# Optimization experiments

Hardware: AMD Instinct MI355X
Metric: run time of the kernel (lower is better)

Reference implementation:

```python
import jax, jax.numpy as jnp
import numpy as np

C = 32
H = 8

def _layernorm(x, scale, bias, eps=1e-5):
    mu = jnp.mean(x, axis=-1, keepdims=True)
    var = jnp.mean(jnp.square(x - mu), axis=-1, keepdims=True)
    return (x - mu) * jax.lax.rsqrt(var + eps) * scale + bias


def setup_inputs() -> dict:
    key = jax.random.key(0)
    ks = jax.random.split(key, 10)
    B, s, i, j = 1, 128, 256, 256
    m = jax.random.normal(ks[0], (B, s, i, C), dtype=jnp.float32)
    z = jax.random.normal(ks[1], (B, i, j, C), dtype=jnp.float32)
    sd = 1.0 / np.sqrt(C)
    return {
        "m": m,
        "z": z,
        "ln_scale": jnp.ones((C,), jnp.float32),
        "ln_bias": jnp.zeros((C,), jnp.float32),
        "lnb_scale": jnp.ones((C,), jnp.float32),
        "lnb_bias": jnp.zeros((C,), jnp.float32),
        "wq": jax.random.normal(ks[2], (C, C * H), jnp.float32) * sd,
        "wk": jax.random.normal(ks[3], (C, C * H), jnp.float32) * sd,
        "wv": jax.random.normal(ks[4], (C, C * H), jnp.float32) * sd,
        "wb": jax.random.normal(ks[5], (C, H), jnp.float32) * sd,
        "wg": jax.random.normal(ks[6], (C, C * H), jnp.float32) * sd,
        "wo": jax.random.normal(ks[7], (C * H, C), jnp.float32) * (1.0 / np.sqrt(C * H)),
        "bo": jnp.zeros((C,), jnp.float32),
    }


def reference(m, z, ln_scale, ln_bias, lnb_scale, lnb_bias, wq, wk, wv, wb, wg, wo, bo):
    B, s, i, _ = m.shape
    j = z.shape[2]
    mn = _layernorm(m, ln_scale, ln_bias)                      # (B,s,i,c)
    q = (mn @ wq).reshape(B, s, i, H, C)                        # (B,s,i,h,c)
    k = (mn @ wk).reshape(B, s, i, H, C)
    v = (mn @ wv).reshape(B, s, i, H, C)
    gate = jax.nn.sigmoid(mn @ wg).reshape(B, s, i, H, C)       # (B,s,i,h,c)
    b = (_layernorm(z, lnb_scale, lnb_bias) @ wb)               # (B,i,j,h)
    a = jnp.einsum('bsihc,bsjhc->bsijh', q, k) * (C ** -0.5) + b[:, None]
    a = jax.nn.softmax(a, axis=-2)                              # softmax over j
    o = gate * jnp.einsum('bsijh,bsjhc->bsihc', a, v)
    o = o.reshape(B, s, i, H * C)
    return o @ wo + bo
```

## Files before the change

kernel.cpp:

```cpp
#include <hip/hip_runtime.h>

constexpr int NC = 32;
constexpr int NH = 8;
constexpr int NS = 128;
constexpr int NI = 256;
constexpr int NJ = 256;
constexpr float LN_EPS = 1e-5f;
constexpr float QSCALE = 0.17677669529663687f;
constexpr float LOG2E  = 1.4426950408889634f;

typedef __bf16 bf16x8 __attribute__((ext_vector_type(8)));
typedef __bf16 bf16x2 __attribute__((ext_vector_type(2)));
typedef float floatx4 __attribute__((ext_vector_type(4)));

__device__ __forceinline__ float fexp2(float x) {
#if __has_builtin(__builtin_amdgcn_exp2f)
    return __builtin_amdgcn_exp2f(x);
#else
    return exp2f(x);
#endif
}
__device__ __forceinline__ float frcp(float x) {
#if __has_builtin(__builtin_amdgcn_rcpf)
    return __builtin_amdgcn_rcpf(x);
#else
    return 1.0f / x;
#endif
}
__device__ __forceinline__ unsigned pk2c(float a, float b) {
    union { bf16x2 v; unsigned u; } c;
    c.v = bf16x2{(__bf16)a, (__bf16)b};
    return c.u;
}

__device__ __forceinline__ int qkOff(int row, int chunk) {
    return row * 32 + ((chunk ^ ((row >> 1) & 3)) << 3);
}
__device__ __forceinline__ int vOff(int c, int chunk) {
    return c * 256 + ((chunk ^ (c & 7)) << 3);
}
__device__ __forceinline__ int pOff(int base, int row, int chunk) {
    return base + row * 32 + ((chunk ^ ((row >> 1) & 3)) << 3);
}

__global__ __launch_bounds__(256) void biasprep_kernel(
    const float* __restrict__ z, const float* __restrict__ lnb_s,
    const float* __restrict__ lnb_b, const float* __restrict__ wb,
    const float* __restrict__ wq, const float* __restrict__ wk,
    const float* __restrict__ wv, const float* __restrict__ wg,
    const float* __restrict__ wo,
    float* __restrict__ bias32, unsigned short* __restrict__ wprep,
    unsigned short* __restrict__ wofrag)
{
    const int b = blockIdx.x;
    const int t = threadIdx.x;
    if (b < 256) {
        const int w_ = b >> 6;
        const int it = (b >> 4) & 3;
        const int jc = (b >> 1) & 7;
        const int jt = b & 1;
        const int lm = (t >> 2) & 15;
        const int lq = t >> 6, r = t & 3;
        const int i = w_ * 64 + it * 16 + lm;
        const int j = jc * 32 + jt * 16 + lq * 4 + r;

        const float4* zr = (const float4*)(z + ((size_t)i * NJ + j) * NC);
        float x[NC];
#pragma unroll
        for (int k = 0; k < 8; ++k) {
            float4 v = zr[k];
            x[4*k] = v.x; x[4*k+1] = v.y; x[4*k+2] = v.z; x[4*k+3] = v.w;
        }
        float mu = 0.f;
#pragma unroll
        for (int c = 0; c < NC; ++c) mu += x[c];
        mu *= (1.0f / NC);
        float var = 0.f;
#pragma unroll
        for (int c = 0; c < NC; ++c) { float d = x[c] - mu; var += d * d; }
        var *= (1.0f / NC);
        float rs = rsqrtf(var + LN_EPS);
        float acc[NH];
#pragma unroll
        for (int h = 0; h < NH; ++h) acc[h] = 0.f;
#pragma unroll
        for (int c = 0; c < NC; ++c) {
            float xn = (x[c] - mu) * rs * lnb_s[c] + lnb_b[c];
#pragma unroll
            for (int h = 0; h < NH; ++h) acc[h] += xn * wb[c * NH + h];
        }
        const int base = jc * 8192 + w_ * 2048 + (jt * 4 + it) * 256 + t;
#pragma unroll
        for (int h = 0; h < NH; ++h)
            bias32[h * 65536 + base] = acc[h] * LOG2E;
    } else if (b < 272) {
        int g = (b - 256) * 256 + t;
        int p  = g >> 10;
        int h  = (g >> 7) & 7;
        int ct = (g >> 6) & 1;
        int l  = g & 63;
        const float* W = (p == 0) ? wq : (p == 1) ? wk : (p == 2) ? wv : wg;
        float scale = (p == 0) ? QSCALE * LOG2E : (p == 3) ? LOG2E : 1.0f;
        int col = 32 * h + 16 * ct + (l & 15);
        int r0  = 8 * (l >> 4);
        float v[8];
#pragma unroll
        for (int e = 0; e < 8; ++e) v[e] = W[(r0 + e) * 256 + col] * scale;
        uint4 u;
        u.x = pk2c(v[0], v[1]); u.y = pk2c(v[2], v[3]);
        u.z = pk2c(v[4], v[5]); u.w = pk2c(v[6], v[7]);
        *(uint4*)&wprep[g * 8] = u;
    } else {
        int g = (b - 272) * 256 + t;
        int tile = g >> 6;
        int l = g & 63;
        int kt = tile >> 1, nt = tile & 1;
        int r0 = kt * 32 + 8 * (l >> 4);
        int col = nt * 16 + (l & 15);
        float v[8];
#pragma unroll
        for (int e = 0; e < 8; ++e) v[e] = wo[(r0 + e) * 32 + col];
        uint4 u;
        u.x = pk2c(v[0], v[1]); u.y = pk2c(v[2], v[3]);
        u.z = pk2c(v[4], v[5]); u.w = pk2c(v[6], v[7]);
        *(uint4*)&wofrag[g * 8] = u;
    }
}

__global__ __launch_bounds__(256, 3) void attn_kernel(
    const float* __restrict__ m, const float* __restrict__ ln_s,
    const float* __restrict__ ln_b,
    const unsigned short* __restrict__ wprep,
    const float* __restrict__ bias32,
    unsigned short* __restrict__ attn16)
{
    __shared__ unsigned short KX[256 * 32];
    __shared__ unsigned short Vt[32 * 256];
    __shared__ unsigned short Pbuf[4 * 2048];

    const int t = threadIdx.x;
    const int h = blockIdx.x & 7;
    const int s = blockIdx.x >> 3;
    const int l = t & 63, w = t >> 6;
    const int lm = l & 15, lq = l >> 4;
    const int ibase = w * 64;
    const int pwb = w * 2048;
    const floatx4 zero = {0.f, 0.f, 0.f, 0.f};

    {
        const float4* mr = (const float4*)(m + ((size_t)s * NI + t) * NC);
        float x[NC];
#pragma unroll
        for (int k = 0; k < 8; ++k) {
            float4 v = mr[k];
            x[4*k] = v.x; x[4*k+1] = v.y; x[4*k+2] = v.z; x[4*k+3] = v.w;
        }
        float mu = 0.f;
#pragma unroll
        for (int c = 0; c < NC; ++c) mu += x[c];
        mu *= (1.0f / NC);
        float var = 0.f;
#pragma unroll
        for (int c = 0; c < NC; ++c) { float d = x[c] - mu; var += d * d; }
        var *= (1.0f / NC);
        float rs = rsqrtf(var + LN_EPS);
#pragma unroll
        for (int k = 0; k < 4; ++k) {
            uint4 u;
            u.x = pk2c((x[8*k+0]-mu)*rs*ln_s[8*k+0]+ln_b[8*k+0],
                       (x[8*k+1]-mu)*rs*ln_s[8*k+1]+ln_b[8*k+1]);
            u.y = pk2c((x[8*k+2]-mu)*rs*ln_s[8*k+2]+ln_b[8*k+2],
                       (x[8*k+3]-mu)*rs*ln_s[8*k+3]+ln_b[8*k+3]);
            u.z = pk2c((x[8*k+4]-mu)*rs*ln_s[8*k+4]+ln_b[8*k+4],
                       (x[8*k+5]-mu)*rs*ln_s[8*k+5]+ln_b[8*k+5]);
            u.w = pk2c((x[8*k+6]-mu)*rs*ln_s[8*k+6]+ln_b[8*k+6],
                       (x[8*k+7]-mu)*rs*ln_s[8*k+7]+ln_b[8*k+7]);
            *(uint4*)&KX[qkOff(t, k)] = u;
        }
    }

    const unsigned short* wp = wprep + ((size_t)h * 128 + l) * 8;
    bf16x8 wfQ[2], wfK[2], wfV[2];
#pragma unroll
    for (int ct = 0; ct < 2; ++ct) {
        wfQ[ct] = *(const bf16x8*)&wp[(0 * 1024 + ct * 64) * 8];
        wfK[ct] = *(const bf16x8*)&wp[(1 * 1024 + ct * 64) * 8];
        wfV[ct] = *(const bf16x8*)&wp[(2 * 1024 + ct * 64) * 8];
    }
    bf16x8 Xb[4];
#pragma unroll
    for (int it = 0; it < 4; ++it)
        Xb[it] = *(const bf16x8*)&KX[qkOff(ibase + it * 16 + lm, lq)];

#pragma unroll
    for (int it = 0; it < 4; ++it)
#pragma unroll
        for (int ct = 0; ct < 2; ++ct) {
            floatx4 d = __builtin_amdgcn_mfma_f32_16x16x32_bf16(wfQ[ct], Xb[it], zero, 0, 0, 0);
            uint2 u; u.x = pk2c(d[0], d[1]); u.y = pk2c(d[2], d[3]);
            int row = ibase + it * 16 + lm;
            *(uint2*)&KX[qkOff(row, 2 * ct + (lq >> 1)) + (lq & 1) * 4] = u;
        }
    bf16x8 Qb[4];
#pragma unroll
    for (int it = 0; it < 4; ++it)
        Qb[it] = *(const bf16x8*)&KX[qkOff(ibase + it * 16 + lm, lq)];

#pragma unroll
    for (int it = 0; it < 4; ++it)
#pragma unroll
        for (int ct = 0; ct < 2; ++ct) {
            floatx4 d = __builtin_amdgcn_mfma_f32_16x16x32_bf16(wfK[ct], Xb[it], zero, 0, 0, 0);
            uint2 u; u.x = pk2c(d[0], d[1]); u.y = pk2c(d[2], d[3]);
            int row = ibase + it * 16 + lm;
            *(uint2*)&KX[qkOff(row, 2 * ct + (lq >> 1)) + (lq & 1) * 4] = u;
        }

#pragma unroll
    for (int jt = 0; jt < 4; ++jt)
#pragma unroll
        for (int ct = 0; ct < 2; ++ct) {
            floatx4 d = __builtin_amdgcn_mfma_f32_16x16x32_bf16(Xb[jt], wfV[ct], zero, 0, 0, 0);
            uint2 u; u.x = pk2c(d[0], d[1]); u.y = pk2c(d[2], d[3]);
            int c = ct * 16 + lm;
            int chunk = 8 * w + 2 * jt + (lq >> 1);
            *(uint2*)&Vt[vOff(c, chunk) + (lq & 1) * 4] = u;
        }

    __syncthreads();

    floatx4 accO[2][4];
#pragma unroll
    for (int ct = 0; ct < 2; ++ct)
#pragma unroll
        for (int it = 0; it < 4; ++it) accO[ct][it] = zero;
    float accLv[4] = {0.f, 0.f, 0.f, 0.f};

    const float* bptr = bias32 + (size_t)h * 65536 + w * 2048 + l * 4;

    for (int jc = 0; jc < 8; ++jc) {
        const float* bj = bptr + jc * 8192;

        floatx4 Cre[4][2];
#pragma unroll
        for (int it = 0; it < 4; ++it) {
            Cre[it][0] = *(const floatx4*)(bj + it * 256);
            Cre[it][1] = *(const floatx4*)(bj + (4 + it) * 256);
        }
        bf16x8 Ka0 = *(const bf16x8*)&KX[qkOff(jc * 32 + lm, lq)];
        bf16x8 Ka1 = *(const bf16x8*)&KX[qkOff(jc * 32 + 16 + lm, lq)];
        bf16x8 Va0 = *(const bf16x8*)&Vt[vOff(lm, 4 * jc + lq)];
        bf16x8 Va1 = *(const bf16x8*)&Vt[vOff(16 + lm, 4 * jc + lq)];

#pragma unroll
        for (int it = 0; it < 4; ++it) {
            const int pb = pwb + it * 512;
            floatx4 S0 = __builtin_amdgcn_mfma_f32_16x16x32_bf16(Ka0, Qb[it], Cre[it][0], 0, 0, 0);
            floatx4 S1 = __builtin_amdgcn_mfma_f32_16x16x32_bf16(Ka1, Qb[it], Cre[it][1], 0, 0, 0);
            float p0 = fexp2(S0[0]), p1 = fexp2(S0[1]);
            float p2 = fexp2(S0[2]), p3 = fexp2(S0[3]);
            float p4 = fexp2(S1[0]), p5 = fexp2(S1[1]);
            float p6 = fexp2(S1[2]), p7 = fexp2(S1[3]);
            accLv[it] += ((p0 + p1) + (p2 + p3)) + ((p4 + p5) + (p6 + p7));
            uint2 u0; u0.x = pk2c(p0, p1); u0.y = pk2c(p2, p3);
            uint2 u1; u1.x = pk2c(p4, p5); u1.y = pk2c(p6, p7);
            *(uint2*)&Pbuf[pOff(pb, lm, 0 + (lq >> 1)) + (lq & 1) * 4] = u0;
            *(uint2*)&Pbuf[pOff(pb, lm, 2 + (lq >> 1)) + (lq & 1) * 4] = u1;
        }

        bf16x8 Pb0 = *(const bf16x8*)&Pbuf[pOff(pwb + 0 * 512, lm, lq)];
        bf16x8 Pb1 = *(const bf16x8*)&Pbuf[pOff(pwb + 1 * 512, lm, lq)];
        bf16x8 Pb2 = *(const bf16x8*)&Pbuf[pOff(pwb + 2 * 512, lm, lq)];
        bf16x8 Pb3 = *(const bf16x8*)&Pbuf[pOff(pwb + 3 * 512, lm, lq)];
        accO[0][0] = __builtin_amdgcn_mfma_f32_16x16x32_bf16(Va0, Pb0, accO[0][0], 0, 0, 0);
        accO[1][0] = __builtin_amdgcn_mfma_f32_16x16x32_bf16(Va1, Pb0, accO[1][0], 0, 0, 0);
        accO[0][1] = __builtin_amdgcn_mfma_f32_16x16x32_bf16(Va0, Pb1, accO[0][1], 0, 0, 0);
        accO[1][1] = __builtin_amdgcn_mfma_f32_16x16x32_bf16(Va1, Pb1, accO[1][1], 0, 0, 0);
        accO[0][2] = __builtin_amdgcn_mfma_f32_16x16x32_bf16(Va0, Pb2, accO[0][2], 0, 0, 0);
        accO[1][2] = __builtin_amdgcn_mfma_f32_16x16x32_bf16(Va1, Pb2, accO[1][2], 0, 0, 0);
        accO[0][3] = __builtin_amdgcn_mfma_f32_16x16x32_bf16(Va0, Pb3, accO[0][3], 0, 0, 0);
        accO[1][3] = __builtin_amdgcn_mfma_f32_16x16x32_bf16(Va1, Pb3, accO[1][3], 0, 0, 0);
    }

    {
        bf16x8 wfG0 = *(const bf16x8*)&wp[(3 * 1024 + 0 * 64) * 8];
        bf16x8 wfG1 = *(const bf16x8*)&wp[(3 * 1024 + 1 * 64) * 8];
#pragma unroll
        for (int it = 0; it < 4; ++it) {
            float L = accLv[it];
            L += __shfl_xor(L, 16, 64);
            L += __shfl_xor(L, 32, 64);
            const float inv = frcp(L);
            floatx4 d0 = __builtin_amdgcn_mfma_f32_16x16x32_bf16(wfG0, Xb[it], zero, 0, 0, 0);
            floatx4 d1 = __builtin_amdgcn_mfma_f32_16x16x32_bf16(wfG1, Xb[it], zero, 0, 0, 0);
            const int tile16 = s * 16 + (w * 4 + it);
            unsigned short* ab = attn16 + ((size_t)(tile16 * 8 + h)) * 512;
            const int lo = lm * 8 + (lq & 1) * 4;
            {
                float o0 = accO[0][it][0] * inv * frcp(1.0f + fexp2(-d0[0]));
                float o1 = accO[0][it][1] * inv * frcp(1.0f + fexp2(-d0[1]));
                float o2 = accO[0][it][2] * inv * frcp(1.0f + fexp2(-d0[2]));
                float o3 = accO[0][it][3] * inv * frcp(1.0f + fexp2(-d0[3]));
                uint2 u; u.x = pk2c(o0, o1); u.y = pk2c(o2, o3);
                *(uint2*)&ab[(0 + (lq >> 1)) * 128 + lo] = u;
            }
            {
                float o0 = accO[1][it][0] * inv * frcp(1.0f + fexp2(-d1[0]));
                float o1 = accO[1][it][1] * inv * frcp(1.0f + fexp2(-d1[1]));
                float o2 = accO[1][it][2] * inv * frcp(1.0f + fexp2(-d1[2]));
                float o3 = accO[1][it][3] * inv * frcp(1.0f + fexp2(-d1[3]));
                uint2 u; u.x = pk2c(o0, o1); u.y = pk2c(o2, o3);
                *(uint2*)&ab[(2 + (lq >> 1)) * 128 + lo] = u;
            }
        }
    }
}

__global__ __launch_bounds__(256) void proj_kernel(
    const unsigned short* __restrict__ attn16,
    const unsigned short* __restrict__ wofrag,
    const float* __restrict__ bo, float* __restrict__ out)
{
    const int t = threadIdx.x;
    const int l = t & 63, w = t >> 6;
    const int lm = l & 15, lq = l >> 4;
    const int row0 = blockIdx.x * 128 + w * 32;
    const int t16 = row0 >> 4;
    const floatx4 zero = {0.f, 0.f, 0.f, 0.f};

    floatx4 acc[2][2];
#pragma unroll
    for (int it = 0; it < 2; ++it)
#pragma unroll
        for (int nt = 0; nt < 2; ++nt) acc[it][nt] = zero;

#pragma unroll 2
    for (int kt = 0; kt < 8; ++kt) {
        bf16x8 a0 = *(const bf16x8*)&attn16[((size_t)((t16 + 0) * 8 + kt)) * 512 + l * 8];
        bf16x8 a1 = *(const bf16x8*)&attn16[((size_t)((t16 + 1) * 8 + kt)) * 512 + l * 8];
        bf16x8 b0 = *(const bf16x8*)&wofrag[((kt * 2 + 0) * 64 + l) * 8];
        bf16x8 b1 = *(const bf16x8*)&wofrag[((kt * 2 + 1) * 64 + l) * 8];
        acc[0][0] = __builtin_amdgcn_mfma_f32_16x16x32_bf16(a0, b0, acc[0][0], 0, 0, 0);
        acc[0][1] = __builtin_amdgcn_mfma_f32_16x16x32_bf16(a0, b1, acc[0][1], 0, 0, 0);
        acc[1][0] = __builtin_amdgcn_mfma_f32_16x16x32_bf16(a1, b0, acc[1][0], 0, 0, 0);
        acc[1][1] = __builtin_amdgcn_mfma_f32_16x16x32_bf16(a1, b1, acc[1][1], 0, 0, 0);
    }

    float bov[2] = {bo[lm], bo[16 + lm]};
#pragma unroll
    for (int it = 0; it < 2; ++it)
#pragma unroll
        for (int nt = 0; nt < 2; ++nt)
#pragma unroll
            for (int r = 0; r < 4; ++r)
                out[(size_t)(row0 + it * 16 + lq * 4 + r) * NC + nt * 16 + lm]
                    = acc[it][nt][r] + bov[nt];
}

extern "C" void kernel_launch(void* const* d_in, const int* in_sizes, int n_in,
                              void* d_out, int out_size, void* d_ws, size_t ws_size,
                              hipStream_t stream) {
    const float* m     = (const float*)d_in[0];
    const float* z     = (const float*)d_in[1];
    const float* ln_s  = (const float*)d_in[2];
    const float* ln_b  = (const float*)d_in[3];
    const float* lnb_s = (const float*)d_in[4];
    const float* lnb_b = (const float*)d_in[5];
    const float* wq    = (const float*)d_in[6];
    const float* wk    = (const float*)d_in[7];
    const float* wv    = (const float*)d_in[8];
    const float* wb    = (const float*)d_in[9];
    const float* wg    = (const float*)d_in[10];
    const float* wo    = (const float*)d_in[11];
    const float* bo    = (const float*)d_in[12];
    float* out = (float*)d_out;

    float* bias32 = (float*)d_ws;
    unsigned short* wprep  = (unsigned short*)((char*)d_ws + (2u << 20));
    unsigned short* wofrag = (unsigned short*)((char*)d_ws + (2u << 20) + 65536);
    unsigned short* attn16 = (unsigned short*)((char*)d_ws + (2u << 20) + 65536 + 16384);

    biasprep_kernel<<<276, 256, 0, stream>>>(z, lnb_s, lnb_b, wb, wq, wk, wv, wg,
                                             wo, bias32, wprep, wofrag);
    attn_kernel<<<NS * NH, 256, 0, stream>>>(m, ln_s, ln_b, wprep, bias32, attn16);
    proj_kernel<<<(NS * NI) / 128, 256, 0, stream>>>(attn16, wofrag, bo, out);
}
```

Measured before the change: 116.8 us.

## Fuse three kernels into one persistent kernel with grid barriers

Replaces the bias-prep, attention and projection launches with a single persistent kernel of 512 blocks that runs the phases back to back, separated by atomic-counter grid barriers. Attention work units are looped over the fixed grid, and the output projection is split so each block handles 64 rows. The aim is to remove kernel launch gaps and tail effects between stages. In exchange it adds a memset launch, spin-wait barrier cost, and occupancy lowered to 2 blocks per SM. It also relies on all 512 blocks being co-resident, otherwise the barrier deadlocks.

```diff
diff --git a/kernel.cpp b/kernel.cpp
--- a/kernel.cpp
+++ b/kernel.cpp
@@ -8,6 +8,7 @@
 constexpr float LN_EPS = 1e-5f;
 constexpr float QSCALE = 0.17677669529663687f;
 constexpr float LOG2E  = 1.4426950408889634f;
+constexpr unsigned GRIDN = 512;
 
 typedef __bf16 bf16x8 __attribute__((ext_vector_type(8)));
 typedef __bf16 bf16x2 __attribute__((ext_vector_type(2)));
@@ -43,26 +44,50 @@
     return base + row * 32 + ((chunk ^ ((row >> 1) & 3)) << 3);
 }
 
-__global__ __launch_bounds__(256) void biasprep_kernel(
-    const float* __restrict__ z, const float* __restrict__ lnb_s,
-    const float* __restrict__ lnb_b, const float* __restrict__ wb,
+__device__ __forceinline__ void grid_barrier(unsigned* ctr) {
+    __syncthreads();
+    if (threadIdx.x == 0) {
+        __threadfence();
+        __hip_atomic_fetch_add(ctr, 1u, __ATOMIC_ACQ_REL, __HIP_MEMORY_SCOPE_AGENT);
+        while (__hip_atomic_load(ctr, __ATOMIC_ACQUIRE, __HIP_MEMORY_SCOPE_AGENT) < GRIDN) {
+            __builtin_amdgcn_s_sleep(2);
+        }
+        __threadfence();
+    }
+    __syncthreads();
+}
+
+__global__ __launch_bounds__(256, 2) void fused_kernel(
+    const float* __restrict__ m, const float* __restrict__ z,
+    const float* __restrict__ ln_s, const float* __restrict__ ln_b,
+    const float* __restrict__ lnb_s, const float* __restrict__ lnb_b,
     const float* __restrict__ wq, const float* __restrict__ wk,
-    const float* __restrict__ wv, const float* __restrict__ wg,
-    const float* __restrict__ wo,
+    const float* __restrict__ wv, const float* __restrict__ wb,
+    const float* __restrict__ wg, const float* __restrict__ wo,
+    const float* __restrict__ bo,
     float* __restrict__ bias32, unsigned short* __restrict__ wprep,
-    unsigned short* __restrict__ wofrag)
+    unsigned short* __restrict__ wofrag, unsigned short* __restrict__ attn16,
+    unsigned* __restrict__ bars, float* __restrict__ out)
 {
-    const int b = blockIdx.x;
+    __shared__ unsigned short KX[256 * 32];
+    __shared__ unsigned short Vt[32 * 256];
+    __shared__ unsigned short Pbuf[4 * 2048];
+
+    const int bid = blockIdx.x;
     const int t = threadIdx.x;
-    if (b < 256) {
-        const int w_ = b >> 6;
-        const int it = (b >> 4) & 3;
-        const int jc = (b >> 1) & 7;
-        const int jt = b & 1;
-        const int lm = (t >> 2) & 15;
-        const int lq = t >> 6, r = t & 3;
-        const int i = w_ * 64 + it * 16 + lm;
-        const int j = jc * 32 + jt * 16 + lq * 4 + r;
+    const int l = t & 63, w = t >> 6;
+    const int lm = l & 15, lq = l >> 4;
+    const floatx4 zero = {0.f, 0.f, 0.f, 0.f};
+
+    if (bid < 256) {
+        const int w_ = bid >> 6;
+        const int it = (bid >> 4) & 3;
+        const int jc = (bid >> 1) & 7;
+        const int jt = bid & 1;
+        const int blm = (t >> 2) & 15;
+        const int blq = t >> 6, br = t & 3;
+        const int i = w_ * 64 + it * 16 + blm;
+        const int j = jc * 32 + jt * 16 + blq * 4 + br;
 
         const float4* zr = (const float4*)(z + ((size_t)i * NJ + j) * NC);
         float x[NC];
@@ -93,16 +118,16 @@
 #pragma unroll
         for (int h = 0; h < NH; ++h)
             bias32[h * 65536 + base] = acc[h] * LOG2E;
-    } else if (b < 272) {
-        int g = (b - 256) * 256 + t;
+    } else if (bid < 272) {
+        int g = (bid - 256) * 256 + t;
         int p  = g >> 10;
         int h  = (g >> 7) & 7;
         int ct = (g >> 6) & 1;
-        int l  = g & 63;
+        int ll = g & 63;
         const float* W = (p == 0) ? wq : (p == 1) ? wk : (p == 2) ? wv : wg;
         float scale = (p == 0) ? QSCALE * LOG2E : (p == 3) ? LOG2E : 1.0f;
-        int col = 32 * h + 16 * ct + (l & 15);
-        int r0  = 8 * (l >> 4);
+        int col = 32 * h + 16 * ct + (ll & 15);
+        int r0  = 8 * (ll >> 4);
         float v[8];
 #pragma unroll
         for (int e = 0; e < 8; ++e) v[e] = W[(r0 + e) * 256 + col] * scale;
@@ -110,13 +135,13 @@
         u.x = pk2c(v[0], v[1]); u.y = pk2c(v[2], v[3]);
         u.z = pk2c(v[4], v[5]); u.w = pk2c(v[6], v[7]);
         *(uint4*)&wprep[g * 8] = u;
-    } else {
-        int g = (b - 272) * 256 + t;
+    } else if (bid < 276) {
+        int g = (bid - 272) * 256 + t;
         int tile = g >> 6;
-        int l = g & 63;
+        int ll = g & 63;
         int kt = tile >> 1, nt = tile & 1;
-        int r0 = kt * 32 + 8 * (l >> 4);
-        int col = nt * 16 + (l & 15);
+        int r0 = kt * 32 + 8 * (ll >> 4);
+        int col = nt * 16 + (ll & 15);
         float v[8];
 #pragma unroll
         for (int e = 0; e < 8; ++e) v[e] = wo[(r0 + e) * 32 + col];
@@ -125,236 +150,210 @@
         u.z = pk2c(v[4], v[5]); u.w = pk2c(v[6], v[7]);
         *(uint4*)&wofrag[g * 8] = u;
     }
-}
-
-__global__ __launch_bounds__(256, 3) void attn_kernel(
-    const float* __restrict__ m, const float* __restrict__ ln_s,
-    const float* __restrict__ ln_b,
-    const unsigned short* __restrict__ wprep,
-    const float* __restrict__ bias32,
-    unsigned short* __restrict__ attn16)
-{
-    __shared__ unsigned short KX[256 * 32];
-    __shared__ unsigned short Vt[32 * 256];
-    __shared__ unsigned short Pbuf[4 * 2048];
-
-    const int t = threadIdx.x;
-    const int h = blockIdx.x & 7;
-    const int s = blockIdx.x >> 3;
-    const int l = t & 63, w = t >> 6;
-    const int lm = l & 15, lq = l >> 4;
-    const int ibase = w * 64;
-    const int pwb = w * 2048;
-    const floatx4 zero = {0.f, 0.f, 0.f, 0.f};
+
+    grid_barrier(&bars[0]);
+
+    for (int u = bid; u < NS * NH; u += GRIDN) {
+        const int h = u & 7;
+        const int s = u >> 3;
+        const int ibase = w * 64;
+        const int pwb = w * 2048;
+
+        __syncthreads();
+
+        {
+            const float4* mr = (const float4*)(m + ((size_t)s * NI + t) * NC);
+            float x[NC];
+#pragma unroll
+            for (int k = 0; k < 8; ++k) {
+                float4 v = mr[k];
+                x[4*k] = v.x; x[4*k+1] = v.y; x[4*k+2] = v.z; x[4*k+3] = v.w;
+            }
+            float mu = 0.f;
+#pragma unroll
+            for (int c = 0; c < NC; ++c) mu += x[c];
+            mu *= (1.0f / NC);
+            float var = 0.f;
+#pragma unroll
+            for (int c = 0; c < NC; ++c) { float d = x[c] - mu; var += d * d; }
+            var *= (1.0f / NC);
+            float rs = rsqrtf(var + LN_EPS);
+#pragma unroll
+            for (int k = 0; k < 4; ++k) {
+                uint4 uu;
+                uu.x = pk2c((x[8*k+0]-mu)*rs*ln_s[8*k+0]+ln_b[8*k+0],
+                            (x[8*k+1]-mu)*rs*ln_s[8*k+1]+ln_b[8*k+1]);
+                uu.y = pk2c((x[8*k+2]-mu)*rs*ln_s[8*k+2]+ln_b[8*k+2],
+                            (x[8*k+3]-mu)*rs*ln_s[8*k+3]+ln_b[8*k+3]);
+                uu.z = pk2c((x[8*k+4]-mu)*rs*ln_s[8*k+4]+ln_b[8*k+4],
+                            (x[8*k+5]-mu)*rs*ln_s[8*k+5]+ln_b[8*k+5]);
+                uu.w = pk2c((x[8*k+6]-mu)*rs*ln_s[8*k+6]+ln_b[8*k+6],
+                            (x[8*k+7]-mu)*rs*ln_s[8*k+7]+ln_b[8*k+7]);
+                *(uint4*)&KX[qkOff(t, k)] = uu;
+            }
+        }
+
+        const unsigned short* wp = wprep + ((size_t)h * 128 + l) * 8;
+        bf16x8 wfQ[2], wfK[2], wfV[2];
+#pragma unroll
+        for (int ct = 0; ct < 2; ++ct) {
+            wfQ[ct] = *(const bf16x8*)&wp[(0 * 1024 + ct * 64) * 8];
+            wfK[ct] = *(const bf16x8*)&wp[(1 * 1024 + ct * 64) * 8];
+            wfV[ct] = *(const bf16x8*)&wp[(2 * 1024 + ct * 64) * 8];
+        }
+        bf16x8 Xb[4];
+#pragma unroll
+        for (int it = 0; it < 4; ++it)
+            Xb[it] = *(const bf16x8*)&KX[qkOff(ibase + it * 16 + lm, lq)];
+
+#pragma unroll
+        for (int it = 0; it < 4; ++it)
+#pragma unroll
+            for (int ct = 0; ct < 2; ++ct) {
+                floatx4 d = __builtin_amdgcn_mfma_f32_16x16x32_bf16(wfQ[ct], Xb[it], zero, 0, 0, 0);
+                uint2 uu; uu.x = pk2c(d[0], d[1]); uu.y = pk2c(d[2], d[3]);
+                int row = ibase + it * 16 + lm;
+                *(uint2*)&KX[qkOff(row, 2 * ct + (lq >> 1)) + (lq & 1) * 4] = uu;
+            }
+        bf16x8 Qb[4];
+#pragma unroll
+        for (int it = 0; it < 4; ++it)
+            Qb[it] = *(const bf16x8*)&KX[qkOff(ibase + it * 16 + lm, lq)];
+
+#pragma unroll
+        for (int it = 0; it < 4; ++it)
+#pragma unroll
+            for (int ct = 0; ct < 2; ++ct) {
+                floatx4 d = __builtin_amdgcn_mfma_f32_16x16x32_bf16(wfK[ct], Xb[it], zero, 0, 0, 0);
+                uint2 uu; uu.x = pk2c(d[0], d[1]); uu.y = pk2c(d[2], d[3]);
+                int row = ibase + it * 16 + lm;
+                *(uint2*)&KX[qkOff(row, 2 * ct + (lq >> 1)) + (lq & 1) * 4] = uu;
+            }
+
+#pragma unroll
+        for (int jt = 0; jt < 4; ++jt)
+#pragma unroll
+            for (int ct = 0; ct < 2; ++ct) {
+                floatx4 d = __builtin_amdgcn_mfma_f32_16x16x32_bf16(Xb[jt], wfV[ct], zero, 0, 0, 0);
+                uint2 uu; uu.x = pk2c(d[0], d[1]); uu.y = pk2c(d[2], d[3]);
+                int c = ct * 16 + lm;
+                int chunk = 8 * w + 2 * jt + (lq >> 1);
+                *(uint2*)&Vt[vOff(c, chunk) + (lq & 1) * 4] = uu;
+            }
+
+        __syncthreads();
+
+        floatx4 accO[2][4];
+#pragma unroll
+        for (int ct = 0; ct < 2; ++ct)
+#pragma unroll
+            for (int it = 0; it < 4; ++it) accO[ct][it] = zero;
+        float accLv[4] = {0.f, 0.f, 0.f, 0.f};
+
+        const float* bptr = bias32 + (size_t)h * 65536 + w * 2048 + l * 4;
+
+        for (int jc = 0; jc < 8; ++jc) {
+            const float* bj = bptr + jc * 8192;
+
+            floatx4 Cre[4][2];
+#pragma unroll
+            for (int it = 0; it < 4; ++it) {
+                Cre[it][0] = *(const floatx4*)(bj + it * 256);
+                Cre[it][1] = *(const floatx4*)(bj + (4 + it) * 256);
+            }
+            bf16x8 Ka0 = *(const bf16x8*)&KX[qkOff(jc * 32 + lm, lq)];
+            bf16x8 Ka1 = *(const bf16x8*)&KX[qkOff(jc * 32 + 16 + lm, lq)];
+            bf16x8 Va0 = *(const bf16x8*)&Vt[vOff(lm, 4 * jc + lq)];
+            bf16x8 Va1 = *(const bf16x8*)&Vt[vOff(16 + lm, 4 * jc + lq)];
+
+#pragma unroll
+            for (int it = 0; it < 4; ++it) {
+                const int pb = pwb + it * 512;
+                floatx4 S0 = __builtin_amdgcn_mfma_f32_16x16x32_bf16(Ka0, Qb[it], Cre[it][0], 0, 0, 0);
+                floatx4 S1 = __builtin_amdgcn_mfma_f32_16x16x32_bf16(Ka1, Qb[it], Cre[it][1], 0, 0, 0);
+                float p0 = fexp2(S0[0]), p1 = fexp2(S0[1]);
+                float p2 = fexp2(S0[2]), p3 = fexp2(S0[3]);
+                float p4 = fexp2(S1[0]), p5 = fexp2(S1[1]);
+                float p6 = fexp2(S1[2]), p7 = fexp2(S1[3]);
+                accLv[it] += ((p0 + p1) + (p2 + p3)) + ((p4 + p5) + (p6 + p7));
+                uint2 u0; u0.x = pk2c(p0, p1); u0.y = pk2c(p2, p3);
+                uint2 u1; u1.x = pk2c(p4, p5); u1.y = pk2c(p6, p7);
+                *(uint2*)&Pbuf[pOff(pb, lm, 0 + (lq >> 1)) + (lq & 1) * 4] = u0;
+                *(uint2*)&Pbuf[pOff(pb, lm, 2 + (lq >> 1)) + (lq & 1) * 4] = u1;
+            }
+
+            bf16x8 Pb0 = *(const bf16x8*)&Pbuf[pOff(pwb + 0 * 512, lm, lq)];
+            bf16x8 Pb1 = *(const bf16x8*)&Pbuf[pOff(pwb + 1 * 512, lm, lq)];
+            bf16x8 Pb2 = *(const bf16x8*)&Pbuf[pOff(pwb + 2 * 512, lm, lq)];
+            bf16x8 Pb3 = *(const bf16x8*)&Pbuf[pOff(pwb + 3 * 512, lm, lq)];
+            accO[0][0] = __builtin_amdgcn_mfma_f32_16x16x32_bf16(Va0, Pb0, accO[0][0], 0, 0, 0);
+            accO[1][0] = __builtin_amdgcn_mfma_f32_16x16x32_bf16(Va1, Pb0, accO[1][0], 0, 0, 0);
+            accO[0][1] = __builtin_amdgcn_mfma_f32_16x16x32_bf16(Va0, Pb1, accO[0][1], 0, 0, 0);
+            accO[1][1] = __builtin_amdgcn_mfma_f32_16x16x32_bf16(Va1, Pb1, accO[1][1], 0, 0, 0);
+            accO[0][2] = __builtin_amdgcn_mfma_f32_16x16x32_bf16(Va0, Pb2, accO[0][2], 0, 0, 0);
+            accO[1][2] = __builtin_amdgcn_mfma_f32_16x16x32_bf16(Va1, Pb2, accO[1][2], 0, 0, 0);
+            accO[0][3] = __builtin_amdgcn_mfma_f32_16x16x32_bf16(Va0, Pb3, accO[0][3], 0, 0, 0);
+            accO[1][3] = __builtin_amdgcn_mfma_f32_16x16x32_bf16(Va1, Pb3, accO[1][3], 0, 0, 0);
+        }
+
+        {
+            bf16x8 wfG0 = *(const bf16x8*)&wp[(3 * 1024 + 0 * 64) * 8];
+            bf16x8 wfG1 = *(const bf16x8*)&wp[(3 * 1024 + 1 * 64) * 8];
+#pragma unroll
+            for (int it = 0; it < 4; ++it) {
+                float L = accLv[it];
+                L += __shfl_xor(L, 16, 64);
+                L += __shfl_xor(L, 32, 64);
+                const float inv = frcp(L);
+                floatx4 d0 = __builtin_amdgcn_mfma_f32_16x16x32_bf16(wfG0, Xb[it], zero, 0, 0, 0);
+                floatx4 d1 = __builtin_amdgcn_mfma_f32_16x16x32_bf16(wfG1, Xb[it], zero, 0, 0, 0);
+                const int tile16 = s * 16 + (w * 4 + it);
+                unsigned short* ab = attn16 + ((size_t)(tile16 * 8 + h)) * 512;
+                const int lo = lm * 8 + (lq & 1) * 4;
+                {
+                    float o0 = accO[0][it][0] * inv * frcp(1.0f + fexp2(-d0[0]));
+                    float o1 = accO[0][it][1] * inv * frcp(1.0f + fexp2(-d0[1]));
+                    float o2 = accO[0][it][2] * inv * frcp(1.0f + fexp2(-d0[2]));
+                    float o3 = accO[0][it][3] * inv * frcp(1.0f + fexp2(-d0[3]));
+                    uint2 uu; uu.x = pk2c(o0, o1); uu.y = pk2c(o2, o3);
+                    *(uint2*)&ab[(0 + (lq >> 1)) * 128 + lo] = uu;
+                }
+                {
+                    float o0 = accO[1][it][0] * inv * frcp(1.0f + fexp2(-d1[0]));
+                    float o1 = accO[1][it][1] * inv * frcp(1.0f + fexp2(-d1[1]));
+                    float o2 = accO[1][it][2] * inv * frcp(1.0f + fexp2(-d1[2]));
+                    float o3 = accO[1][it][3] * inv * frcp(1.0f + fexp2(-d1[3]));
+                    uint2 uu; uu.x = pk2c(o0, o1); uu.y = pk2c(o2, o3);
+                    *(uint2*)&ab[(2 + (lq >> 1)) * 128 + lo] = uu;
+                }
+            }
+        }
+    }
+
+    grid_barrier(&bars[1]);
 
     {
-        const float4* mr = (const float4*)(m + ((size_t)s * NI + t) * NC);
-        float x[NC];
-#pragma unroll
-        for (int k = 0; k < 8; ++k) {
-            float4 v = mr[k];
-            x[4*k] = v.x; x[4*k+1] = v.y; x[4*k+2] = v.z; x[4*k+3] = v.w;
-        }
-        float mu = 0.f;
-#pragma unroll
-        for (int c = 0; c < NC; ++c) mu += x[c];
-        mu *= (1.0f / NC);
-        float var = 0.f;
-#pragma unroll
-        for (int c = 0; c < NC; ++c) { float d = x[c] - mu; var += d * d; }
-        var *= (1.0f / NC);
-        float rs = rsqrtf(var + LN_EPS);
-#pragma unroll
-        for (int k = 0; k < 4; ++k) {
-            uint4 u;
-            u.x = pk2c((x[8*k+0]-mu)*rs*ln_s[8*k+0]+ln_b[8*k+0],
-                       (x[8*k+1]-mu)*rs*ln_s[8*k+1]+ln_b[8*k+1]);
-            u.y = pk2c((x[8*k+2]-mu)*rs*ln_s[8*k+2]+ln_b[8*k+2],
-                       (x[8*k+3]-mu)*rs*ln_s[8*k+3]+ln_b[8*k+3]);
-            u.z = pk2c((x[8*k+4]-mu)*rs*ln_s[8*k+4]+ln_b[8*k+4],
-                       (x[8*k+5]-mu)*rs*ln_s[8*k+5]+ln_b[8*k+5]);
-            u.w = pk2c((x[8*k+6]-mu)*rs*ln_s[8*k+6]+ln_b[8*k+6],
-                       (x[8*k+7]-mu)*rs*ln_s[8*k+7]+ln_b[8*k+7]);
-            *(uint4*)&KX[qkOff(t, k)] = u;
-        }
+        const int row0 = bid * 64 + w * 16;
+        const int t16 = bid * 4 + w;
+        floatx4 acc[2] = {zero, zero};
+
+#pragma unroll
+        for (int kt = 0; kt < 8; ++kt) {
+            bf16x8 a0 = *(const bf16x8*)&attn16[((size_t)(t16 * 8 + kt)) * 512 + l * 8];
+            bf16x8 b0 = *(const bf16x8*)&wofrag[((kt * 2 + 0) * 64 + l) * 8];
+            bf16x8 b1 = *(const bf16x8*)&wofrag[((kt * 2 + 1) * 64 + l) * 8];
+            acc[0] = __builtin_amdgcn_mfma_f32_16x16x32_bf16(a0, b0, acc[0], 0, 0, 0);
+            acc[1] = __builtin_amdgcn_mfma_f32_16x16x32_bf16(a0, b1, acc[1], 0, 0, 0);
+        }
+
+        float bov[2] = {bo[lm], bo[16 + lm]};
+#pragma unroll
+        for (int nt = 0; nt < 2; ++nt)
+#pragma unroll
+            for (int r = 0; r < 4; ++r)
+                out[(size_t)(row0 + lq * 4 + r) * NC + nt * 16 + lm]
+                    = acc[nt][r] + bov[nt];
     }
-
-    const unsigned short* wp = wprep + ((size_t)h * 128 + l) * 8;
-    bf16x8 wfQ[2], wfK[2], wfV[2];
-#pragma unroll
-    for (int ct = 0; ct < 2; ++ct) {
-        wfQ[ct] = *(const bf16x8*)&wp[(0 * 1024 + ct * 64) * 8];
-        wfK[ct] = *(const bf16x8*)&wp[(1 * 1024 + ct * 64) * 8];
-        wfV[ct] = *(const bf16x8*)&wp[(2 * 1024 + ct * 64) * 8];
-    }
-    bf16x8 Xb[4];
-#pragma unroll
-    for (int it = 0; it < 4; ++it)
-        Xb[it] = *(const bf16x8*)&KX[qkOff(ibase + it * 16 + lm, lq)];
-
-#pragma unroll
-    for (int it = 0; it < 4; ++it)
-#pragma unroll
-        for (int ct = 0; ct < 2; ++ct) {
-            floatx4 d = __builtin_amdgcn_mfma_f32_16x16x32_bf16(wfQ[ct], Xb[it], zero, 0, 0, 0);
-            uint2 u; u.x = pk2c(d[0], d[1]); u.y = pk2c(d[2], d[3]);
-            int row = ibase + it * 16 + lm;
-            *(uint2*)&KX[qkOff(row, 2 * ct + (lq >> 1)) + (lq & 1) * 4] = u;
-        }
-    bf16x8 Qb[4];
-#pragma unroll
-    for (int it = 0; it < 4; ++it)
-        Qb[it] = *(const bf16x8*)&KX[qkOff(ibase + it * 16 + lm, lq)];
-
-#pragma unroll
-    for (int it = 0; it < 4; ++it)
-#pragma unroll
-        for (int ct = 0; ct < 2; ++ct) {
-            floatx4 d = __builtin_amdgcn_mfma_f32_16x16x32_bf16(wfK[ct], Xb[it], zero, 0, 0, 0);
-            uint2 u; u.x = pk2c(d[0], d[1]); u.y = pk2c(d[2], d[3]);
-            int row = ibase + it * 16 + lm;
-            *(uint2*)&KX[qkOff(row, 2 * ct + (lq >> 1)) + (lq & 1) * 4] = u;
-        }
-
-#pragma unroll
-    for (int jt = 0; jt < 4; ++jt)
-#pragma unroll
-        for (int ct = 0; ct < 2; ++ct) {
-            floatx4 d = __builtin_amdgcn_mfma_f32_16x16x32_bf16(Xb[jt], wfV[ct], zero, 0, 0, 0);
-            uint2 u; u.x = pk2c(d[0], d[1]); u.y = pk2c(d[2], d[3]);
-            int c = ct * 16 + lm;
-            int chunk = 8 * w + 2 * jt + (lq >> 1);
-            *(uint2*)&Vt[vOff(c, chunk) + (lq & 1) * 4] = u;
-        }
-
-    __syncthreads();
-
-    floatx4 accO[2][4];
-#pragma unroll
-    for (int ct = 0; ct < 2; ++ct)
-#pragma unroll
-        for (int it = 0; it < 4; ++it) accO[ct][it] = zero;
-    float accLv[4] = {0.f, 0.f, 0.f, 0.f};
-
-    const float* bptr = bias32 + (size_t)h * 65536 + w * 2048 + l * 4;
-
-    for (int jc = 0; jc < 8; ++jc) {
-        const float* bj = bptr + jc * 8192;
-
-        floatx4 Cre[4][2];
-#pragma unroll
-        for (int it = 0; it < 4; ++it) {
-            Cre[it][0] = *(const floatx4*)(bj + it * 256);
-            Cre[it][1] = *(const floatx4*)(bj + (4 + it) * 256);
-        }
-        bf16x8 Ka0 = *(const bf16x8*)&KX[qkOff(jc * 32 + lm, lq)];
-        bf16x8 Ka1 = *(const bf16x8*)&KX[qkOff(jc * 32 + 16 + lm, lq)];
-        bf16x8 Va0 = *(const bf16x8*)&Vt[vOff(lm, 4 * jc + lq)];
-        bf16x8 Va1 = *(const bf16x8*)&Vt[vOff(16 + lm, 4 * jc + lq)];
-
-#pragma unroll
-        for (int it = 0; it < 4; ++it) {
-            const int pb = pwb + it * 512;
-            floatx4 S0 = __builtin_amdgcn_mfma_f32_16x16x32_bf16(Ka0, Qb[it], Cre[it][0], 0, 0, 0);
-            floatx4 S1 = __builtin_amdgcn_mfma_f32_16x16x32_bf16(Ka1, Qb[it], Cre[it][1], 0, 0, 0);
-            float p0 = fexp2(S0[0]), p1 = fexp2(S0[1]);
-            float p2 = fexp2(S0[2]), p3 = fexp2(S0[3]);
-            float p4 = fexp2(S1[0]), p5 = fexp2(S1[1]);
-            float p6 = fexp2(S1[2]), p7 = fexp2(S1[3]);
-            accLv[it] += ((p0 + p1) + (p2 + p3)) + ((p4 + p5) + (p6 + p7));
-            uint2 u0; u0.x = pk2c(p0, p1); u0.y = pk2c(p2, p3);
-            uint2 u1; u1.x = pk2c(p4, p5); u1.y = pk2c(p6, p7);
-            *(uint2*)&Pbuf[pOff(pb, lm, 0 + (lq >> 1)) + (lq & 1) * 4] = u0;
-            *(uint2*)&Pbuf[pOff(pb, lm, 2 + (lq >> 1)) + (lq & 1) * 4] = u1;
-        }
-
-        bf16x8 Pb0 = *(const bf16x8*)&Pbuf[pOff(pwb + 0 * 512, lm, lq)];
-        bf16x8 Pb1 = *(const bf16x8*)&Pbuf[pOff(pwb + 1 * 512, lm, lq)];
-        bf16x8 Pb2 = *(const bf16x8*)&Pbuf[pOff(pwb + 2 * 512, lm, lq)];
-        bf16x8 Pb3 = *(const bf16x8*)&Pbuf[pOff(pwb + 3 * 512, lm, lq)];
-        accO[0][0] = __builtin_amdgcn_mfma_f32_16x16x32_bf16(Va0, Pb0, accO[0][0], 0, 0, 0);
-        accO[1][0] = __builtin_amdgcn_mfma_f32_16x16x32_bf16(Va1, Pb0, accO[1][0], 0, 0, 0);
-        accO[0][1] = __builtin_amdgcn_mfma_f32_16x16x32_bf16(Va0, Pb1, accO[0][1], 0, 0, 0);
-        accO[1][1] = __builtin_amdgcn_mfma_f32_16x16x32_bf16(Va1, Pb1, accO[1][1], 0, 0, 0);
-        accO[0][2] = __builtin_amdgcn_mfma_f32_16x16x32_bf16(Va0, Pb2, accO[0][2], 0, 0, 0);
-        accO[1][2] = __builtin_amdgcn_mfma_f32_16x16x32_bf16(Va1, Pb2, accO[1][2], 0, 0, 0);
-        accO[0][3] = __builtin_amdgcn_mfma_f32_16x16x32_bf16(Va0, Pb3, accO[0][3], 0, 0, 0);
-        accO[1][3] = __builtin_amdgcn_mfma_f32_16x16x32_bf16(Va1, Pb3, accO[1][3], 0, 0, 0);
-    }
-
-    {
-        bf16x8 wfG0 = *(const bf16x8*)&wp[(3 * 1024 + 0 * 64) * 8];
-        bf16x8 wfG1 = *(const bf16x8*)&wp[(3 * 1024 + 1 * 64) * 8];
-#pragma unroll
-        for (int it = 0; it < 4; ++it) {
-            float L = accLv[it];
-            L += __shfl_xor(L, 16, 64);
-            L += __shfl_xor(L, 32, 64);
-            const float inv = frcp(L);
-            floatx4 d0 = __builtin_amdgcn_mfma_f32_16x16x32_bf16(wfG0, Xb[it], zero, 0, 0, 0);
-            floatx4 d1 = __builtin_amdgcn_mfma_f32_16x16x32_bf16(wfG1, Xb[it], zero, 0, 0, 0);
-            const int tile16 = s * 16 + (w * 4 + it);
-            unsigned short* ab = attn16 + ((size_t)(tile16 * 8 + h)) * 512;
-            const int lo = lm * 8 + (lq & 1) * 4;
-            {
-                float o0 = accO[0][it][0] * inv * frcp(1.0f + fexp2(-d0[0]));
-                float o1 = accO[0][it][1] * inv * frcp(1.0f + fexp2(-d0[1]));
-                float o2 = accO[0][it][2] * inv * frcp(1.0f + fexp2(-d0[2]));
-                float o3 = accO[0][it][3] * inv * frcp(1.0f + fexp2(-d0[3]));
-                uint2 u; u.x = pk2c(o0, o1); u.y = pk2c(o2, o3);
-                *(uint2*)&ab[(0 + (lq >> 1)) * 128 + lo] = u;
-            }
-            {
-                float o0 = accO[1][it][0] * inv * frcp(1.0f + fexp2(-d1[0]));
-                float o1 = accO[1][it][1] * inv * frcp(1.0f + fexp2(-d1[1]));
-                float o2 = accO[1][it][2] * inv * frcp(1.0f + fexp2(-d1[2]));
-                float o3 = accO[1][it][3] * inv * frcp(1.0f + fexp2(-d1[3]));
-                uint2 u; u.x = pk2c(o0, o1); u.y = pk2c(o2, o3);
-                *(uint2*)&ab[(2 + (lq >> 1)) * 128 + lo] = u;
-            }
-        }
-    }
-}
-
-__global__ __launch_bounds__(256) void proj_kernel(
-    const unsigned short* __restrict__ attn16,
-    const unsigned short* __restrict__ wofrag,
-    const float* __restrict__ bo, float* __restrict__ out)
-{
-    const int t = threadIdx.x;
-    const int l = t & 63, w = t >> 6;
-    const int lm = l & 15, lq = l >> 4;
-    const int row0 = blockIdx.x * 128 + w * 32;
-    const int t16 = row0 >> 4;
-    const floatx4 zero = {0.f, 0.f, 0.f, 0.f};
-
-    floatx4 acc[2][2];
-#pragma unroll
-    for (int it = 0; it < 2; ++it)
-#pragma unroll
-        for (int nt = 0; nt < 2; ++nt) acc[it][nt] = zero;
-
-#pragma unroll 2
-    for (int kt = 0; kt < 8; ++kt) {
-        bf16x8 a0 = *(const bf16x8*)&attn16[((size_t)((t16 + 0) * 8 + kt)) * 512 + l * 8];
-        bf16x8 a1 = *(const bf16x8*)&attn16[((size_t)((t16 + 1) * 8 + kt)) * 512 + l * 8];
-        bf16x8 b0 = *(const bf16x8*)&wofrag[((kt * 2 + 0) * 64 + l) * 8];
-        bf16x8 b1 = *(const bf16x8*)&wofrag[((kt * 2 + 1) * 64 + l) * 8];
-        acc[0][0] = __builtin_amdgcn_mfma_f32_16x16x32_bf16(a0, b0, acc[0][0], 0, 0, 0);
-        acc[0][1] = __builtin_amdgcn_mfma_f32_16x16x32_bf16(a0, b1, acc[0][1], 0, 0, 0);
-        acc[1][0] = __builtin_amdgcn_mfma_f32_16x16x32_bf16(a1, b0, acc[1][0], 0, 0, 0);
-        acc[1][1] = __builtin_amdgcn_mfma_f32_16x16x32_bf16(a1, b1, acc[1][1], 0, 0, 0);
-    }
-
-    float bov[2] = {bo[lm], bo[16 + lm]};
-#pragma unroll
-    for (int it = 0; it < 2; ++it)
-#pragma unroll
-        for (int nt = 0; nt < 2; ++nt)
-#pragma unroll
-            for (int r = 0; r < 4; ++r)
-                out[(size_t)(row0 + it * 16 + lq * 4 + r) * NC + nt * 16 + lm]
-                    = acc[it][nt][r] + bov[nt];
 }
 
 extern "C" void kernel_launch(void* const* d_in, const int* in_sizes, int n_in,
@@ -379,9 +378,11 @@
     unsigned short* wprep  = (unsigned short*)((char*)d_ws + (2u << 20));
     unsigned short* wofrag = (unsigned short*)((char*)d_ws + (2u << 20) + 65536);
     unsigned short* attn16 = (unsigned short*)((char*)d_ws + (2u << 20) + 65536 + 16384);
-
-    biasprep_kernel<<<276, 256, 0, stream>>>(z, lnb_s, lnb_b, wb, wq, wk, wv, wg,
-                                             wo, bias32, wprep, wofrag);
-    attn_kernel<<<NS * NH, 256, 0, stream>>>(m, ln_s, ln_b, wprep, bias32, attn16);
-    proj_kernel<<<(NS * NI) / 128, 256, 0, stream>>>(attn16, wofrag, bo, out);
-}
+    unsigned* bars = (unsigned*)((char*)d_ws + (32u << 20));
+
+    hipMemsetAsync(bars, 0, 2 * sizeof(unsigned), stream);
+    fused_kernel<<<GRIDN, 256, 0, stream>>>(m, z, ln_s, ln_b, lnb_s, lnb_b,
+                                            wq, wk, wv, wb, wg, wo, bo,
+                                            bias32, wprep, wofrag, attn16,
+                                            bars, out);
+}
```

After: 273.2 us. 2.34x slower.
